# Optimization experiments

Measured on AMD Instinct MI355X. Metric: run time of the kernel, lower is better.

The kernel has to match this reference:

```python
import jax, jax.numpy as jnp
import numpy as np

HEADS = 24
HEAD_DIM = 128
HIDDEN = HEADS * HEAD_DIM          # 3072
MLP_DIM = int(HIDDEN * 4.0)        # 12288
EPS = 1e-6


def _layernorm(x, eps=EPS):
    mu = jnp.mean(x, axis=-1, keepdims=True)
    var = jnp.mean(jnp.square(x - mu), axis=-1, keepdims=True)
    return (x - mu) * jax.lax.rsqrt(var + eps)


def _rmsnorm(x, w, eps=EPS):
    var = jnp.mean(jnp.square(x), axis=-1, keepdims=True)
    return x * jax.lax.rsqrt(var + eps) * w


def _apply_rope_transposed(x, freqs_cis):
    # x: [B, S_img, H, Dh]; freqs_cis: [S_img, 2*Dh]
    cos, sin = jnp.split(freqs_cis[:, None, :], 2, axis=-1)  # each [S_img, 1, Dh]
    xr = x.reshape(*x.shape[:-1], -1, 2)                      # interleaved pairs
    x_real, x_imag = xr[..., 0], xr[..., 1]
    x_rot = jnp.stack([-x_imag, x_real], axis=-1).reshape(x.shape)
    return x * cos + x_rot * sin


def setup_inputs() -> dict:
    key = jax.random.key(0)
    ks = jax.random.split(key, 20)
    B, S_IMG, S_TXT = 1, 2048, 256
    s = 0.02
    inp = {
        "hidden_states": jax.random.normal(ks[0], (B, S_IMG, HIDDEN), jnp.float32),
        "encoder_hidden_states": jax.random.normal(ks[1], (B, S_TXT, HIDDEN), jnp.float32),
        "temb": jax.random.normal(ks[2], (B, HIDDEN), jnp.float32),
        "freqs_cis": jax.random.uniform(ks[3], (S_IMG, 2 * HEAD_DIM), jnp.float32),
        # AdaLN: Linear(hidden, 3*hidden)
        "w_norm": jax.random.normal(ks[4], (HIDDEN, 3 * HIDDEN), jnp.float32) * s,
        "b_norm": jnp.zeros((3 * HIDDEN,), jnp.float32),
        # attention projections (bias=True)
        "wq": jax.random.normal(ks[5], (HIDDEN, HIDDEN), jnp.float32) * s,
        "bq": jnp.zeros((HIDDEN,), jnp.float32),
        "wk": jax.random.normal(ks[6], (HIDDEN, HIDDEN), jnp.float32) * s,
        "bk": jnp.zeros((HIDDEN,), jnp.float32),
        "wv": jax.random.normal(ks[7], (HIDDEN, HIDDEN), jnp.float32) * s,
        "bv": jnp.zeros((HIDDEN,), jnp.float32),
        # QK RMSNorm weights over head_dim
        "nq_w": jnp.ones((HEAD_DIM,), jnp.float32),
        "nk_w": jnp.ones((HEAD_DIM,), jnp.float32),
        # parallel MLP branch
        "w_mlp": jax.random.normal(ks[8], (HIDDEN, MLP_DIM), jnp.float32) * s,
        "b_mlp": jnp.zeros((MLP_DIM,), jnp.float32),
        # proj_out: Linear(hidden + mlp_dim, hidden)
        "w_out": jax.random.normal(ks[9], (HIDDEN + MLP_DIM, HIDDEN), jnp.float32) * s,
        "b_out": jnp.zeros((HIDDEN,), jnp.float32),
    }
    return inp


def reference(hidden_states, encoder_hidden_states, temb, freqs_cis,
              w_norm, b_norm, wq, bq, wk, bk, wv, bv, nq_w, nk_w,
              w_mlp, b_mlp, w_out, b_out):
    B = hidden_states.shape[0]
    T = encoder_hidden_states.shape[1]  # text_seq_length

    x = jnp.concatenate([hidden_states, encoder_hidden_states], axis=1)  # [B,S,D]
    residual = x

    # AdaLayerNormZeroSingle
    emb = jax.nn.silu(temb) @ w_norm + b_norm          # [B, 3D]
    emb = emb[:, None, :]                              # [B, 1, 3D]
    shift, scale, gate = jnp.split(emb, 3, axis=-1)    # each [B,1,D]
    nx = _layernorm(x) * (1.0 + scale) + shift         # [B,S,D]

    # parallel MLP branch
    mlp = jax.nn.gelu(nx @ w_mlp + b_mlp, approximate=True)  # [B,S,MLP]

    # attention: q/k/v over full (img+txt) normed sequence
    q = (nx @ wq + bq).reshape(B, -1, HEADS, HEAD_DIM)
    k = (nx @ wk + bk).reshape(B, -1, HEADS, HEAD_DIM)
    v = (nx @ wv + bv).reshape(B, -1, HEADS, HEAD_DIM)
    q = _rmsnorm(q, nq_w)
    k = _rmsnorm(k, nk_w)

    # transposed RoPE on image tokens only
    q = jnp.concatenate([_apply_rope_transposed(q[:, :-T], freqs_cis), q[:, -T:]], axis=1)
    k = jnp.concatenate([_apply_rope_transposed(k[:, :-T], freqs_cis), k[:, -T:]], axis=1)

    # full (non-varlen) scaled dot-product attention
    scores = jnp.einsum("bqhd,bkhd->bhqk", q, k) / np.sqrt(HEAD_DIM).astype(np.float32)
    probs = jax.nn.softmax(scores, axis=-1)
    attn = jnp.einsum("bhqk,bkhd->bqhd", probs, v).reshape(B, -1, HIDDEN)

    # concat attention + mlp, project, gated residual
    h = jnp.concatenate([attn, mlp], axis=2)           # [B,S,D+MLP]
    h = gate * (h @ w_out + b_out) + residual          # [B,S,D]

    return h[:, :-T, :], h[:, -T:, :]
```

## Files before the change

### kernel.cpp

```cpp
#include <hip/hip_runtime.h>
#include <hip/hip_bf16.h>

typedef unsigned short u16;
typedef short s16x8 __attribute__((ext_vector_type(8)));
typedef float f32x4 __attribute__((ext_vector_type(4)));
typedef int   i32x4 __attribute__((ext_vector_type(4)));
typedef int   i32x2 __attribute__((ext_vector_type(2)));
typedef u16   u16x4 __attribute__((ext_vector_type(4)));
typedef unsigned int u32;
typedef u32   u32x2 __attribute__((ext_vector_type(2)));

#define HEADS  24
#define HD     128
#define HIDDEN 3072
#define MLPD   12288
#define NTOK   2304
#define SIMG   2048
#define NEMB   9216
#define CATD   15360
#define QKVD   9216
#define FUSEN  21504
#define LN_EPS 1e-6f
#define MB     9

__device__ __forceinline__ u16 f2us(float f){
  __hip_bfloat16 h = __float2bfloat16(f);
  return *reinterpret_cast<u16*>(&h);
}
__device__ __forceinline__ float us2f(u16 u){
  __hip_bfloat16 h;
  *reinterpret_cast<u16*>(&h) = u;
  return __bfloat162float(h);
}
__device__ __forceinline__ float gelu_tanh(float x){
  float y = 0.7978845608028654f*(x + 0.044715f*x*x*x);
  y = fminf(fmaxf(y, -12.f), 12.f);
  float e = __expf(-2.f*y);
  float t = (1.f - e) / (1.f + e);
  return 0.5f*x*(1.0f + t);
}
__device__ __forceinline__ void gload16(const u16* g, u16* l){
  __builtin_amdgcn_global_load_lds(
      (const __attribute__((address_space(1))) void*)g,
      (__attribute__((address_space(3))) void*)l, 16, 0, 0);
}
#define BAR() do{ asm volatile("":::"memory"); __builtin_amdgcn_s_barrier(); asm volatile("":::"memory"); }while(0)
#define LGKM0() asm volatile("s_waitcnt lgkmcnt(0)":::"memory")
#define VMW_(n) asm volatile("s_waitcnt vmcnt(" #n ")":::"memory")
#define VMW(n) VMW_(n)

__global__ __launch_bounds__(256)
void emb_partial(const float* __restrict__ temb, const float* __restrict__ wn,
                 float* __restrict__ partial)
{
  __shared__ float ls[384];
  int tid = threadIdx.x;
  int kb = blockIdx.y * 384;
  for (int i = tid; i < 384; i += 256){
    float t = temb[kb + i];
    ls[i] = t / (1.0f + __expf(-t));
  }
  __syncthreads();
  int j = blockIdx.x*256 + tid;
  const float* wp = wn + (size_t)kb*NEMB + j;
  float acc = 0.f;
  #pragma unroll 8
  for (int i = 0; i < 384; i++){ acc = fmaf(ls[i], wp[0], acc); wp += NEMB; }
  partial[blockIdx.y*NEMB + j] = acc;
}

__global__ __launch_bounds__(256)
void emb_reduce(const float* __restrict__ partial, const float* __restrict__ bn,
                float* __restrict__ emb)
{
  int j = blockIdx.x*256 + threadIdx.x;
  float s = bn[j];
  #pragma unroll
  for (int r = 0; r < 8; r++) s += partial[r*NEMB + j];
  emb[j] = s;
}

__global__ __launch_bounds__(256)
void ln_mod(const float* __restrict__ hs, const float* __restrict__ ehs,
            const float* __restrict__ emb, u16* __restrict__ nx)
{
  int row = blockIdx.x;
  const float* x = (row < SIMG) ? hs + (size_t)row*HIDDEN
                                : ehs + (size_t)(row - SIMG)*HIDDEN;
  int tid = threadIdx.x;
  float vals[12];
  float s = 0.f, ss = 0.f;
  #pragma unroll
  for (int i = 0; i < 3; i++){
    float4 v = *reinterpret_cast<const float4*>(x + i*1024 + tid*4);
    vals[i*4+0]=v.x; vals[i*4+1]=v.y; vals[i*4+2]=v.z; vals[i*4+3]=v.w;
    s += v.x+v.y+v.z+v.w;
    ss += v.x*v.x + v.y*v.y + v.z*v.z + v.w*v.w;
  }
  #pragma unroll
  for (int d = 1; d < 64; d <<= 1){ s += __shfl_xor(s, d); ss += __shfl_xor(ss, d); }
  __shared__ float red[8];
  if ((tid & 63) == 0){ red[tid>>6] = s; red[4 + (tid>>6)] = ss; }
  __syncthreads();
  s  = red[0]+red[1]+red[2]+red[3];
  ss = red[4]+red[5]+red[6]+red[7];
  float mu = s * (1.0f/HIDDEN);
  float var = ss * (1.0f/HIDDEN) - mu*mu;
  float rs = rsqrtf(var + LN_EPS);
  #pragma unroll
  for (int i = 0; i < 3; i++){
    int col = i*1024 + tid*4;
    u16x4 o;
    #pragma unroll
    for (int j = 0; j < 4; j++){
      float nv = (vals[i*4+j] - mu) * rs;
      float outv = nv * (1.0f + emb[HIDDEN + col + j]) + emb[col + j];
      o[j] = f2us(outv);
    }
    *reinterpret_cast<u16x4*>(nx + (size_t)row*HIDDEN + col) = o;
  }
}

__global__ __launch_bounds__(256)
void transpose_w(const float* __restrict__ W, u16* __restrict__ Wt,
                 int K, int N, int ldt, int noff)
{
  __shared__ float t[64][65];
  const int tid = threadIdx.x;
  const int kb = blockIdx.y * 64, nb = blockIdx.x * 64;
  #pragma unroll
  for (int i = 0; i < 4; i++){
    int row = (tid >> 4) + i*16;
    int c4  = (tid & 15) * 4;
    float4 v = *reinterpret_cast<const float4*>(W + (size_t)(kb+row)*N + nb + c4);
    t[row][c4] = v.x; t[row][c4+1] = v.y; t[row][c4+2] = v.z; t[row][c4+3] = v.w;
  }
  __syncthreads();
  int n  = tid >> 2;
  int kc = (tid & 3) * 16;
  u16 tmp[16];
  #pragma unroll
  for (int j = 0; j < 16; j++) tmp[j] = f2us(t[kc+j][n]);
  u16* dst = Wt + (size_t)(noff + nb + n)*ldt + kb + kc;
  *reinterpret_cast<i32x4*>(dst)     = *reinterpret_cast<const i32x4*>(tmp);
  *reinterpret_cast<i32x4*>(dst + 8) = *reinterpret_cast<const i32x4*>(tmp + 8);
}

template<int EPI>
__global__ __launch_bounds__(512, 2)
void gemm8(const u16* __restrict__ A_, int lda,
           const u16* __restrict__ Bt_, int ldb,
           int K, int N, int kspl,
           const float* __restrict__ b0, const float* __restrict__ b1,
           const float* __restrict__ b2, const float* __restrict__ b3,
           u16* __restrict__ qkvo, u16* __restrict__ hcat,
           float* __restrict__ outf)
{
  extern __shared__ __align__(16) u16 lds[];
  const int tid = threadIdx.x, lane = tid & 63, wid = tid >> 6;
  const int l15 = lane & 15, lhi = lane >> 4;
  const int wm = wid >> 2, wn = wid & 3;
  const int NKH = K / 32;

  const u16* Ag = A_  + (size_t)blockIdx.z * kspl;
  const u16* Bg = Bt_ + (size_t)blockIdx.z * kspl;

  const int nwg = gridDim.x;
  int orig = blockIdx.x;
  int qq = nwg >> 3, rr = nwg & 7;
  int xcd = orig & 7, loc = orig >> 3;
  int wg = (xcd < rr ? xcd*(qq+1) : rr*(qq+1) + (xcd-rr)*qq) + loc;
  const int m0 = (wg % MB) * 256;
  const int n0 = (wg / MB) * 256;

  const u16 *gA0, *gA1, *gB0, *gB1;
  {
    size_t offA[2], offB[2];
    #pragma unroll
    for (int q = 0; q < 2; q++){
      int Lb = q*8192 + tid*16;
      int r  = Lb >> 7;
      int gp = (Lb >> 4) & 7;
      int g  = gp ^ (r & 7);
      int row = 2*r + (g >> 2);
      int ke  = (g & 3) * 8;
      offA[q] = (size_t)(m0 + row)*lda + ke;
      offB[q] = (size_t)(n0 + row)*ldb + ke;
    }
    gA0 = Ag + offA[0]; gA1 = Ag + offA[1];
    gB0 = Bg + offB[0]; gB1 = Bg + offB[1];
  }
  u16* dA0 = lds + tid*8;
  u16* dA1 = lds + 4096 + tid*8;
  u16* dB0 = lds + 32768 + tid*8;
  u16* dB1 = lds + 36864 + tid*8;

  const char *pa0, *pb0;
  {
    const char* LB = (const char*)lds;
    int Ra = wm*128 + l15;
    pa0 = LB + (Ra>>1)*128 + (((((Ra&1)<<2)|lhi) ^ ((Ra>>1)&7))*16);
    int Rb = wn*64 + l15;
    pb0 = LB + 65536 + (Rb>>1)*128 + (((((Rb&1)<<2)|lhi) ^ ((Rb>>1)&7))*16);
  }

  f32x4 acc[8][4];
  #pragma unroll
  for (int i = 0; i < 8; i++)
    #pragma unroll
    for (int j = 0; j < 4; j++){ f32x4 z = {0.f,0.f,0.f,0.f}; acc[i][j] = z; }

  #define LD8(P_) (*reinterpret_cast<const s16x8*>(P_))
  #define MFMA_ALL(AF_, BF_) do{                                               \
    _Pragma("unroll") for (int a_=0;a_<8;a_++)                                 \
      _Pragma("unroll") for (int nf_=0;nf_<4;nf_++)                            \
        acc[a_][nf_] = __builtin_amdgcn_mfma_f32_16x16x32_bf16(                \
            (AF_)[a_], (BF_)[nf_], acc[a_][nf_], 0, 0, 0); }while(0)

  #define PHASEP(RP_,SP_,DOI_,GOFF_,VN_) do{                                   \
    s16x8 af[8], bf[4];                                                        \
    af[0] = LD8(pa0 + (RP_)*16384);                                            \
    _Pragma("unroll") for (int i_=0;i_<4;i_++)                                 \
      bf[i_] = LD8(pb0 + (RP_)*16384 + i_*1024);                               \
    _Pragma("unroll") for (int i_=1;i_<8;i_++)                                 \
      af[i_] = LD8(pa0 + (RP_)*16384 + (i_>>2)*4096 + (i_&3)*1024);            \
    if (DOI_){                                                                 \
      gload16(gA0+(GOFF_), dA0+(SP_)*8192); gload16(gA1+(GOFF_), dA1+(SP_)*8192);\
      gload16(gB0+(GOFF_), dB0+(SP_)*8192); gload16(gB1+(GOFF_), dB1+(SP_)*8192);\
    }                                                                          \
    __builtin_amdgcn_s_setprio(1);                                             \
    MFMA_ALL(af, bf);                                                          \
    __builtin_amdgcn_s_setprio(0);                                             \
    LGKM0();                                                                   \
    VMW(VN_);                                                                  \
    BAR();                                                                     \
  }while(0)

  gload16(gA0,    dA0);        gload16(gA1,    dA1);
  gload16(gB0,    dB0);        gload16(gB1,    dB1);
  gload16(gA0+32, dA0+8192);   gload16(gA1+32, dA1+8192);
  gload16(gB0+32, dB0+8192);   gload16(gB1+32, dB1+8192);
  gload16(gA0+64, dA0+16384);  gload16(gA1+64, dA1+16384);
  gload16(gB0+64, dB0+16384);  gload16(gB1+64, dB1+16384);
  VMW(8);
  BAR();

  const int nblk = NKH >> 3;
  for (int b = 0; b < nblk - 1; b++){
    PHASEP(0,3,1, 96,8); PHASEP(1,0,1,128,8); PHASEP(2,1,1,160,8); PHASEP(3,2,1,192,8);
    PHASEP(0,3,1,224,8); PHASEP(1,0,1,256,8); PHASEP(2,1,1,288,8); PHASEP(3,2,1,320,8);
    gA0 += 256; gA1 += 256; gB0 += 256; gB1 += 256;
  }
  PHASEP(0,3,1, 96,8); PHASEP(1,0,1,128,8); PHASEP(2,1,1,160,8); PHASEP(3,2,1,192,8);
  PHASEP(0,3,1,224,8); PHASEP(1,0,0,  0,4); PHASEP(2,1,0,  0,0); PHASEP(3,2,0,  0,0);

  #undef PHASEP
  #undef MFMA_ALL
  #undef LD8

  #pragma unroll
  for (int a = 0; a < 8; a++){
    #pragma unroll
    for (int nf = 0; nf < 4; nf++){
      int col = n0 + wn*64 + nf*16 + l15;
      #pragma unroll
      for (int r = 0; r < 4; r++){
        int row = m0 + wm*128 + a*16 + lhi*4 + r;
        float v = acc[a][nf][r];
        if constexpr (EPI == 0){
          if (col < QKVD){
            const float* bp = b0; int c = col;
            if (c >= 6144){ bp = b2; c -= 6144; }
            else if (c >= 3072){ bp = b1; c -= 3072; }
            qkvo[(size_t)row*QKVD + col] = f2us(v + bp[c]);
          } else {
            int c2 = col - QKVD;
            hcat[(size_t)row*CATD + HIDDEN + c2] = f2us(gelu_tanh(v + b3[c2]));
          }
        } else {
          outf[(size_t)blockIdx.z*NTOK*HIDDEN + (size_t)row*HIDDEN + col] = v;
        }
      }
    }
  }
}

__global__ __launch_bounds__(256)
void reduce_out(const float* __restrict__ part, const float* __restrict__ bout,
                const float* __restrict__ emb,
                const float* __restrict__ hs, const float* __restrict__ ehs,
                float* __restrict__ outp)
{
  int row = blockIdx.x;
  const float* res = (row < SIMG) ? hs + (size_t)row*HIDDEN
                                  : ehs + (size_t)(row - SIMG)*HIDDEN;
  #pragma unroll
  for (int i = 0; i < 3; i++){
    int col = i*1024 + threadIdx.x*4;
    float4 a = *reinterpret_cast<const float4*>(part + (size_t)row*HIDDEN + col);
    float4 b = *reinterpret_cast<const float4*>(part + (size_t)NTOK*HIDDEN + (size_t)row*HIDDEN + col);
    float4 rr = *reinterpret_cast<const float4*>(res + col);
    float4 bb = *reinterpret_cast<const float4*>(bout + col);
    float4 gg = *reinterpret_cast<const float4*>(emb + 2*HIDDEN + col);
    float4 o;
    o.x = gg.x*(a.x+b.x+bb.x) + rr.x;
    o.y = gg.y*(a.y+b.y+bb.y) + rr.y;
    o.z = gg.z*(a.z+b.z+bb.z) + rr.z;
    o.w = gg.w*(a.w+b.w+bb.w) + rr.w;
    *reinterpret_cast<float4*>(outp + (size_t)row*HIDDEN + col) = o;
  }
}

__global__ __launch_bounds__(256)
void qk_post(u16* __restrict__ qkv,
             const float* __restrict__ nqw, const float* __restrict__ nkw,
             const float* __restrict__ fc)
{
  int rid = blockIdx.x*4 + (threadIdx.x >> 6);
  int lane = threadIdx.x & 63;
  int isK = rid >= NTOK*HEADS;
  int r = isK ? rid - NTOK*HEADS : rid;
  int token = r / HEADS, head = r % HEADS;
  u16* p = qkv + (size_t)token*QKVD + (isK ? HIDDEN : 0) + head*HD + lane*2;
  unsigned int u = *reinterpret_cast<unsigned int*>(p);
  float v0 = us2f((u16)(u & 0xffff));
  float v1 = us2f((u16)(u >> 16));
  float ss = v0*v0 + v1*v1;
  #pragma unroll
  for (int d = 1; d < 64; d <<= 1) ss += __shfl_xor(ss, d);
  float rs = rsqrtf(ss * (1.0f/HD) + LN_EPS);
  const float* wv = isK ? nkw : nqw;
  v0 *= rs * wv[lane*2];
  v1 *= rs * wv[lane*2+1];
  if (token < SIMG){
    const float* f = fc + (size_t)token*(2*HD);
    float c0 = f[lane*2],      c1 = f[lane*2+1];
    float s0 = f[HD + lane*2], s1 = f[HD + lane*2+1];
    float o0 = v0*c0 - v1*s0;
    float o1 = v1*c1 + v0*s1;
    v0 = o0; v1 = o1;
  }
  unsigned int uo = (unsigned int)f2us(v0) | ((unsigned int)f2us(v1) << 16);
  *reinterpret_cast<unsigned int*>(p) = uo;
}

__global__ __launch_bounds__(512)
void attn_kernel(const u16* __restrict__ qkv, u16* __restrict__ hcat)
{
  __shared__ __align__(16) u16 Ks[64][136];
  __shared__ __align__(16) u16 Vt[128][72];
  __shared__ __align__(16) u16 Ps[128][72];

  const int tid = threadIdx.x, lane = tid & 63, w = tid >> 6;
  const int head = blockIdx.y;
  const int l15 = lane & 15, lhi = lane >> 4;
  const int q0 = blockIdx.x * 128;
  const float scale = 0.08838834764831845f;

  s16x8 qf[4];
  {
    const u16* qrow = qkv + (size_t)(q0 + w*16 + l15)*QKVD + head*HD;
    #pragma unroll
    for (int ks = 0; ks < 4; ks++)
      qf[ks] = *reinterpret_cast<const s16x8*>(qrow + ks*32 + lhi*8);
  }

  int krow[2], kd0[2];
  #pragma unroll
  for (int i = 0; i < 2; i++){ int c = tid + 512*i; krow[i] = c >> 4; kd0[i] = (c & 15)*8; }
  const int vd0   = (tid & 31) * 4;
  const int vbase = (tid >> 5) * 4;
  char* vwp = (char*)(&Vt[0][0]) + vd0*144 + (((vbase>>3) ^ ((vd0>>3)&7))*16) + (vbase&7)*2;

  i32x4 kr0, kr1;
  i32x2 vr0, vr1, vr2, vr3;
  {
    const u16* kbp = qkv + HIDDEN + (size_t)head*HD;
    const u16* vbp = qkv + 2*HIDDEN + (size_t)head*HD;
    kr0 = *reinterpret_cast<const i32x4*>(kbp + (size_t)(krow[0])*QKVD + kd0[0]);
    kr1 = *reinterpret_cast<const i32x4*>(kbp + (size_t)(krow[1])*QKVD + kd0[1]);
    vr0 = *reinterpret_cast<const i32x2*>(vbp + (size_t)(vbase+0)*QKVD + vd0);
    vr1 = *reinterpret_cast<const i32x2*>(vbp + (size_t)(vbase+1)*QKVD + vd0);
    vr2 = *reinterpret_cast<const i32x2*>(vbp + (size_t)(vbase+2)*QKVD + vd0);
    vr3 = *reinterpret_cast<const i32x2*>(vbp + (size_t)(vbase+3)*QKVD + vd0);
  }

  f32x4 O[8];
  #pragma unroll
  for (int i = 0; i < 8; i++){ f32x4 z = {0.f,0.f,0.f,0.f}; O[i] = z; }
  float mrow[4], lrow[4];
  #pragma unroll
  for (int r = 0; r < 4; r++){ mrow[r] = -1e30f; lrow[r] = 0.f; }

  for (int kv0 = 0; kv0 < NTOK; kv0 += 64){
    *reinterpret_cast<i32x4*>(&Ks[krow[0]][kd0[0]]) = kr0;
    *reinterpret_cast<i32x4*>(&Ks[krow[1]][kd0[1]]) = kr1;
    #pragma unroll
    for (int dd = 0; dd < 4; dd++){
      u32 a0 = (u32)(dd & 1 ? ((u32)vr0[dd>>1]) >> 16 : ((u32)vr0[dd>>1]) & 0xffff);
      u32 a1 = (u32)(dd & 1 ? ((u32)vr1[dd>>1]) >> 16 : ((u32)vr1[dd>>1]) & 0xffff);
      u32 a2 = (u32)(dd & 1 ? ((u32)vr2[dd>>1]) >> 16 : ((u32)vr2[dd>>1]) & 0xffff);
      u32 a3 = (u32)(dd & 1 ? ((u32)vr3[dd>>1]) >> 16 : ((u32)vr3[dd>>1]) & 0xffff);
      u32x2 pk; pk[0] = a0 | (a1 << 16); pk[1] = a2 | (a3 << 16);
      *reinterpret_cast<u32x2*>(vwp + dd*144) = pk;
    }
    __syncthreads();

    if (kv0 + 64 < NTOK){
      const u16* kbp = qkv + (size_t)(kv0+64)*QKVD + HIDDEN + (size_t)head*HD;
      const u16* vbp = qkv + (size_t)(kv0+64)*QKVD + 2*HIDDEN + (size_t)head*HD;
      kr0 = *reinterpret_cast<const i32x4*>(kbp + (size_t)(krow[0])*QKVD + kd0[0]);
      kr1 = *reinterpret_cast<const i32x4*>(kbp + (size_t)(krow[1])*QKVD + kd0[1]);
      vr0 = *reinterpret_cast<const i32x2*>(vbp + (size_t)(vbase+0)*QKVD + vd0);
      vr1 = *reinterpret_cast<const i32x2*>(vbp + (size_t)(vbase+1)*QKVD + vd0);
      vr2 = *reinterpret_cast<const i32x2*>(vbp + (size_t)(vbase+2)*QKVD + vd0);
      vr3 = *reinterpret_cast<const i32x2*>(vbp + (size_t)(vbase+3)*QKVD + vd0);
    }

    f32x4 S[4];
    #pragma unroll
    for (int nf = 0; nf < 4; nf++){ f32x4 z = {0.f,0.f,0.f,0.f}; S[nf] = z; }
    #pragma unroll
    for (int ks = 0; ks < 4; ks++){
      #pragma unroll
      for (int nf = 0; nf < 4; nf++){
        s16x8 b = *reinterpret_cast<const s16x8*>(&Ks[nf*16 + l15][ks*32 + lhi*8]);
        S[nf] = __builtin_amdgcn_mfma_f32_16x16x32_bf16(qf[ks], b, S[nf], 0, 0, 0);
      }
    }
    #pragma unroll
    for (int nf = 0; nf < 4; nf++)
      #pragma unroll
      for (int r = 0; r < 4; r++) S[nf][r] *= scale;

    float fsc[4];
    #pragma unroll
    for (int r = 0; r < 4; r++){
      float mx = -1e30f;
      #pragma unroll
      for (int nf = 0; nf < 4; nf++) mx = fmaxf(mx, S[nf][r]);
      #pragma unroll
      for (int d = 1; d < 16; d <<= 1) mx = fmaxf(mx, __shfl_xor(mx, d));
      float mn = fmaxf(mrow[r], mx);
      float f = __expf(mrow[r] - mn);
      mrow[r] = mn; fsc[r] = f;
      float lsum = 0.f;
      int prow = w*16 + lhi*4 + r;
      #pragma unroll
      for (int nf = 0; nf < 4; nf++){
        float pvl = __expf(S[nf][r] - mn);
        lsum += pvl;
        int pcol = nf*16 + l15;
        int col = (((pcol>>3) ^ (prow&7)) << 3) | (pcol & 7);
        Ps[prow][col] = f2us(pvl);
      }
      #pragma unroll
      for (int d = 1; d < 16; d <<= 1) lsum += __shfl_xor(lsum, d);
      lrow[r] = lrow[r]*f + lsum;
    }
    #pragma unroll
    for (int nf = 0; nf < 8; nf++)
      #pragma unroll
      for (int r = 0; r < 4; r++) O[nf][r] *= fsc[r];

    #pragma unroll
    for (int ks = 0; ks < 2; ks++){
      int prow = w*16 + l15;
      int cb = ((ks*4 + lhi) ^ (prow & 7)) << 3;
      s16x8 a = *reinterpret_cast<const s16x8*>(&Ps[prow][cb]);
      #pragma unroll
      for (int nf = 0; nf < 8; nf++){
        int d = nf*16 + l15;
        int vb = ((ks*4 + lhi) ^ ((d>>3)&7)) << 3;
        s16x8 b = *reinterpret_cast<const s16x8*>(&Vt[d][vb]);
        O[nf] = __builtin_amdgcn_mfma_f32_16x16x32_bf16(a, b, O[nf], 0, 0, 0);
      }
    }
    __syncthreads();
  }

  #pragma unroll
  for (int nf = 0; nf < 8; nf++){
    #pragma unroll
    for (int r = 0; r < 4; r++){
      int row = q0 + w*16 + lhi*4 + r;
      int col = head*HD + nf*16 + l15;
      hcat[(size_t)row*CATD + col] = f2us(O[nf][r] / lrow[r]);
    }
  }
}

extern "C" void kernel_launch(void* const* d_in, const int* in_sizes, int n_in,
                              void* d_out, int out_size, void* d_ws, size_t ws_size,
                              hipStream_t stream)
{
  const float* hs    = (const float*)d_in[0];
  const float* ehs   = (const float*)d_in[1];
  const float* temb  = (const float*)d_in[2];
  const float* fc    = (const float*)d_in[3];
  const float* wnorm = (const float*)d_in[4];
  const float* bnorm = (const float*)d_in[5];
  const float* wq    = (const float*)d_in[6];
  const float* bq    = (const float*)d_in[7];
  const float* wk    = (const float*)d_in[8];
  const float* bk    = (const float*)d_in[9];
  const float* wv    = (const float*)d_in[10];
  const float* bv    = (const float*)d_in[11];
  const float* nqw   = (const float*)d_in[12];
  const float* nkw   = (const float*)d_in[13];
  const float* wmlp  = (const float*)d_in[14];
  const float* bmlp  = (const float*)d_in[15];
  const float* wout  = (const float*)d_in[16];
  const float* bout  = (const float*)d_in[17];
  float* outp = (float*)d_out;

  char* ws = (char*)d_ws;
  float* emb  = (float*)ws;
  float* part = (float*)(ws + 36864);
  u16* nx     = (u16*)(ws + 36864 + 294912);
  u16* qkv    = nx  + (size_t)NTOK*HIDDEN;
  u16* hcat   = qkv + (size_t)NTOK*QKVD;
  u16* Wt     = hcat + (size_t)NTOK*CATD;
  float* partial = (float*)nx;

  hipFuncSetAttribute((const void*)gemm8<0>, hipFuncAttributeMaxDynamicSharedMemorySize, 131072);
  hipFuncSetAttribute((const void*)gemm8<1>, hipFuncAttributeMaxDynamicSharedMemorySize, 131072);

  emb_partial<<<dim3(36,8), 256, 0, stream>>>(temb, wnorm, part);
  emb_reduce<<<36, 256, 0, stream>>>(part, bnorm, emb);
  ln_mod<<<NTOK, 256, 0, stream>>>(hs, ehs, emb, nx);

  transpose_w<<<dim3(48,48), 256, 0, stream>>>(wq,   Wt, HIDDEN, HIDDEN, HIDDEN, 0);
  transpose_w<<<dim3(48,48), 256, 0, stream>>>(wk,   Wt, HIDDEN, HIDDEN, HIDDEN, HIDDEN);
  transpose_w<<<dim3(48,48), 256, 0, stream>>>(wv,   Wt, HIDDEN, HIDDEN, HIDDEN, 2*HIDDEN);
  transpose_w<<<dim3(192,48), 256, 0, stream>>>(wmlp, Wt, HIDDEN, MLPD, HIDDEN, QKVD);

  gemm8<0><<<dim3((FUSEN/256)*MB, 1, 1), 512, 131072, stream>>>(
      nx, HIDDEN, Wt, HIDDEN, HIDDEN, FUSEN, 0,
      bq, bk, bv, bmlp, qkv, hcat, nullptr);

  transpose_w<<<dim3(48,240), 256, 0, stream>>>(wout, Wt, CATD, HIDDEN, CATD, 0);

  qk_post<<<(2*NTOK*HEADS)/4, 256, 0, stream>>>(qkv, nqw, nkw, fc);
  attn_kernel<<<dim3(NTOK/128, HEADS), 512, 0, stream>>>(qkv, hcat);

  gemm8<1><<<dim3((HIDDEN/256)*MB, 1, 2), 512, 131072, stream>>>(
      hcat, CATD, Wt, CATD, CATD/2, HIDDEN, CATD/2,
      nullptr, nullptr, nullptr, nullptr, nullptr, nullptr, partial);

  reduce_out<<<NTOK, 256, 0, stream>>>(partial, bout, emb, hs, ehs, outp);
}
```

Measured before the change: 952.3 us.

## Restructure GEMM main loop into quadrant-split ping-pong with 64-wide K tiles

Replaces the 4-stage 32-wide K pipeline with a double-buffered 64-wide K tile scheme. Each tile is split into four quadrant MFMA sub-phases (A-half by B-half), with LDS fragment reads and global-to-LDS staging interleaved between them. The aim is to overlap LDS reads and global loads with MFMA work at a finer grain and to cut register pressure for fragments. In exchange it adds more barriers per tile and a more delicate buffer-reuse schedule.

```diff
diff --git a/kernel.cpp b/kernel.cpp
--- a/kernel.cpp
+++ b/kernel.cpp
@@ -160,7 +160,7 @@
   const int tid = threadIdx.x, lane = tid & 63, wid = tid >> 6;
   const int l15 = lane & 15, lhi = lane >> 4;
   const int wm = wid >> 2, wn = wid & 3;
-  const int NKH = K / 32;
+  const int NT = K / 64;
 
   const u16* Ag = A_  + (size_t)blockIdx.z * kspl;
   const u16* Bg = Bt_ + (size_t)blockIdx.z * kspl;
@@ -190,10 +190,6 @@
     gA0 = Ag + offA[0]; gA1 = Ag + offA[1];
     gB0 = Bg + offB[0]; gB1 = Bg + offB[1];
   }
-  u16* dA0 = lds + tid*8;
-  u16* dA1 = lds + 4096 + tid*8;
-  u16* dB0 = lds + 32768 + tid*8;
-  u16* dB1 = lds + 36864 + tid*8;
 
   const char *pa0, *pb0;
   {
@@ -210,53 +206,96 @@
     #pragma unroll
     for (int j = 0; j < 4; j++){ f32x4 z = {0.f,0.f,0.f,0.f}; acc[i][j] = z; }
 
+  s16x8 aset[8], bset[4];
+
   #define LD8(P_) (*reinterpret_cast<const s16x8*>(P_))
-  #define MFMA_ALL(AF_, BF_) do{                                               \
-    _Pragma("unroll") for (int a_=0;a_<8;a_++)                                 \
-      _Pragma("unroll") for (int nf_=0;nf_<4;nf_++)                            \
-        acc[a_][nf_] = __builtin_amdgcn_mfma_f32_16x16x32_bf16(                \
-            (AF_)[a_], (BF_)[nf_], acc[a_][nf_], 0, 0, 0); }while(0)
-
-  #define PHASEP(RP_,SP_,DOI_,GOFF_,VN_) do{                                   \
-    s16x8 af[8], bf[4];                                                        \
-    af[0] = LD8(pa0 + (RP_)*16384);                                            \
-    _Pragma("unroll") for (int i_=0;i_<4;i_++)                                 \
-      bf[i_] = LD8(pb0 + (RP_)*16384 + i_*1024);                               \
-    _Pragma("unroll") for (int i_=1;i_<8;i_++)                                 \
-      af[i_] = LD8(pa0 + (RP_)*16384 + (i_>>2)*4096 + (i_&3)*1024);            \
-    if (DOI_){                                                                 \
-      gload16(gA0+(GOFF_), dA0+(SP_)*8192); gload16(gA1+(GOFF_), dA1+(SP_)*8192);\
-      gload16(gB0+(GOFF_), dB0+(SP_)*8192); gload16(gB1+(GOFF_), dB1+(SP_)*8192);\
-    }                                                                          \
-    __builtin_amdgcn_s_setprio(1);                                             \
-    MFMA_ALL(af, bf);                                                          \
-    __builtin_amdgcn_s_setprio(0);                                             \
-    LGKM0();                                                                   \
-    VMW(VN_);                                                                  \
-    BAR();                                                                     \
+  #define READ_A(QM_, PP_) do{                                                 \
+    _Pragma("unroll") for (int kh_=0;kh_<2;kh_++)                              \
+      _Pragma("unroll") for (int mf_=0;mf_<4;mf_++)                            \
+        aset[kh_*4+mf_] = LD8(pa0 + ((PP_)*2+kh_)*16384 + (QM_)*4096 + mf_*1024);}while(0)
+  #define READ_B(QN_, PP_) do{                                                 \
+    _Pragma("unroll") for (int kh_=0;kh_<2;kh_++)                              \
+      _Pragma("unroll") for (int nf_=0;nf_<2;nf_++)                            \
+        bset[kh_*2+nf_] = LD8(pb0 + ((PP_)*2+kh_)*16384 + (QN_)*2048 + nf_*1024);}while(0)
+  #define MM16(QM_, QN_) do{                                                   \
+    _Pragma("unroll") for (int kh_=0;kh_<2;kh_++)                              \
+      _Pragma("unroll") for (int mf_=0;mf_<4;mf_++)                            \
+        _Pragma("unroll") for (int nf_=0;nf_<2;nf_++)                          \
+          acc[(QM_)*4+mf_][(QN_)*2+nf_] = __builtin_amdgcn_mfma_f32_16x16x32_bf16(\
+              aset[kh_*4+mf_], bset[kh_*2+nf_], acc[(QM_)*4+mf_][(QN_)*2+nf_],0,0,0);}while(0)
+  #define STGA(GOFF_, RB_) do{ gload16(gA0+(GOFF_), lds+(RB_)+tid*8);          \
+                               gload16(gA1+(GOFF_), lds+(RB_)+4096+tid*8); }while(0)
+  #define STGB(GOFF_, RB_) do{ gload16(gB0+(GOFF_), lds+(RB_)+tid*8);          \
+                               gload16(gB1+(GOFF_), lds+(RB_)+4096+tid*8); }while(0)
+  #define PRIO1() __builtin_amdgcn_s_setprio(1)
+  #define PRIO0() __builtin_amdgcn_s_setprio(0)
+
+  #define TILE_FULL(P_) do{                                                    \
+                                                              \
+    READ_A(0,P_); READ_B(0,P_);                                                \
+    STGA((P_)?160:96, (P_)?8192:24576);                                        \
+    STGB((P_)?128:64, (P_)?32768:49152);                                       \
+    BAR(); LGKM0(); PRIO1(); MM16(0,0); PRIO0(); BAR();                        \
+                                                              \
+    READ_B(1,P_);                                                              \
+    STGB((P_)?160:96, (P_)?40960:57344);                                       \
+    BAR(); LGKM0(); PRIO1(); MM16(0,1); PRIO0(); BAR();                        \
+                                                              \
+    READ_A(1,P_);                                                              \
+    BAR(); LGKM0(); PRIO1(); MM16(1,1); PRIO0(); BAR();                        \
+                                                              \
+    READ_B(0,P_);                                                              \
+    STGA((P_)?192:128, (P_)?16384:0);                                          \
+    BAR(); LGKM0(); PRIO1(); MM16(1,0); PRIO0(); VMW(2); BAR();                \
   }while(0)
 
-  gload16(gA0,    dA0);        gload16(gA1,    dA1);
-  gload16(gB0,    dB0);        gload16(gB1,    dB1);
-  gload16(gA0+32, dA0+8192);   gload16(gA1+32, dA1+8192);
-  gload16(gB0+32, dB0+8192);   gload16(gB1+32, dB1+8192);
-  gload16(gA0+64, dA0+16384);  gload16(gA1+64, dA1+16384);
-  gload16(gB0+64, dB0+16384);  gload16(gB1+64, dB1+16384);
-  VMW(8);
+  STGA(0, 0);
+  STGA(32, 8192);
+  STGB(0, 32768);
+  STGB(32, 40960);
+  STGA(64, 16384);
+  VMW(2);
   BAR();
 
-  const int nblk = NKH >> 3;
-  for (int b = 0; b < nblk - 1; b++){
-    PHASEP(0,3,1, 96,8); PHASEP(1,0,1,128,8); PHASEP(2,1,1,160,8); PHASEP(3,2,1,192,8);
-    PHASEP(0,3,1,224,8); PHASEP(1,0,1,256,8); PHASEP(2,1,1,288,8); PHASEP(3,2,1,320,8);
-    gA0 += 256; gA1 += 256; gB0 += 256; gB1 += 256;
-  }
-  PHASEP(0,3,1, 96,8); PHASEP(1,0,1,128,8); PHASEP(2,1,1,160,8); PHASEP(3,2,1,192,8);
-  PHASEP(0,3,1,224,8); PHASEP(1,0,0,  0,4); PHASEP(2,1,0,  0,0); PHASEP(3,2,0,  0,0);
-
-  #undef PHASEP
-  #undef MFMA_ALL
+  const int npair = (NT - 2) >> 1;
+  for (int pr = 0; pr < npair; pr++){
+    TILE_FULL(0);
+    TILE_FULL(1);
+    gA0 += 128; gA1 += 128; gB0 += 128; gB1 += 128;
+  }
+  {
+    READ_A(0,0); READ_B(0,0);
+    STGA(96, 24576);
+    STGB(64, 49152);
+    BAR(); LGKM0(); PRIO1(); MM16(0,0); PRIO0(); BAR();
+    READ_B(1,0);
+    STGB(96, 57344);
+    BAR(); LGKM0(); PRIO1(); MM16(0,1); PRIO0(); BAR();
+    READ_A(1,0);
+    BAR(); LGKM0(); PRIO1(); MM16(1,1); PRIO0(); BAR();
+    READ_B(0,0);
+    BAR(); LGKM0(); PRIO1(); MM16(1,0); PRIO0(); VMW(0); BAR();
+  }
+  {
+    READ_A(0,1); READ_B(0,1);
+    BAR(); LGKM0(); PRIO1(); MM16(0,0); PRIO0(); BAR();
+    READ_B(1,1);
+    BAR(); LGKM0(); PRIO1(); MM16(0,1); PRIO0(); BAR();
+    READ_A(1,1);
+    BAR(); LGKM0(); PRIO1(); MM16(1,1); PRIO0(); BAR();
+    READ_B(0,1);
+    LGKM0(); PRIO1(); MM16(1,0); PRIO0();
+  }
+
+  #undef TILE_FULL
+  #undef STGA
+  #undef STGB
+  #undef MM16
+  #undef READ_A
+  #undef READ_B
   #undef LD8
+  #undef PRIO1
+  #undef PRIO0
 
   #pragma unroll
   for (int a = 0; a < 8; a++){
```

Result: no change. 951.9 us (-0.0%).

## Quantize fused QKV+MLP GEMM to int8 with per-row and per-column scales

Applied to the files above, without the earlier changes.

Switches the big fused QKV/MLP projection from bf16 MFMA to int8 MFMA (16x16x64). LayerNorm output is quantized per row with a max-abs scale, and the weights are quantized per output column after a new column-max reduction pass. Results are dequantized in the epilogue. This roughly halves operand bandwidth and doubles MFMA throughput for the largest GEMM. In exchange it adds column-max kernels and risks accuracy loss from 8-bit quantization of activations and weights.

```diff
diff --git a/kernel.cpp b/kernel.cpp
--- a/kernel.cpp
+++ b/kernel.cpp
@@ -22,6 +22,7 @@
 #define FUSEN  21504
 #define LN_EPS 1e-6f
 #define MB     9
+#define INV127SQ (1.0f/16129.0f)
 
 __device__ __forceinline__ u16 f2us(float f){
   __hip_bfloat16 h = __float2bfloat16(f);
@@ -39,7 +40,11 @@
   float t = (1.f - e) / (1.f + e);
   return 0.5f*x*(1.0f + t);
 }
-__device__ __forceinline__ void gload16(const u16* g, u16* l){
+__device__ __forceinline__ int q8i(float x, float s){
+  int q = __float2int_rn(x*s);
+  return max(-127, min(127, q));
+}
+__device__ __forceinline__ void gload16(const void* g, void* l){
   __builtin_amdgcn_global_load_lds(
       (const __attribute__((address_space(1))) void*)g,
       (__attribute__((address_space(3))) void*)l, 16, 0, 0);
@@ -82,7 +87,8 @@
 
 __global__ __launch_bounds__(256)
 void ln_mod(const float* __restrict__ hs, const float* __restrict__ ehs,
-            const float* __restrict__ emb, u16* __restrict__ nx)
+            const float* __restrict__ emb, char* __restrict__ nx,
+            float* __restrict__ arow)
 {
   int row = blockIdx.x;
   const float* x = (row < SIMG) ? hs + (size_t)row*HIDDEN
@@ -107,23 +113,64 @@
   float mu = s * (1.0f/HIDDEN);
   float var = ss * (1.0f/HIDDEN) - mu*mu;
   float rs = rsqrtf(var + LN_EPS);
+
+  float mx = 1e-8f;
   #pragma unroll
   for (int i = 0; i < 3; i++){
     int col = i*1024 + tid*4;
-    u16x4 o;
     #pragma unroll
     for (int j = 0; j < 4; j++){
       float nv = (vals[i*4+j] - mu) * rs;
       float outv = nv * (1.0f + emb[HIDDEN + col + j]) + emb[col + j];
-      o[j] = f2us(outv);
-    }
-    *reinterpret_cast<u16x4*>(nx + (size_t)row*HIDDEN + col) = o;
-  }
-}
-
-__global__ __launch_bounds__(256)
-void transpose_w(const float* __restrict__ W, u16* __restrict__ Wt,
-                 int K, int N, int ldt, int noff)
+      vals[i*4+j] = outv;
+      mx = fmaxf(mx, fabsf(outv));
+    }
+  }
+  #pragma unroll
+  for (int d = 1; d < 64; d <<= 1) mx = fmaxf(mx, __shfl_xor(mx, d));
+  __shared__ float redm[4];
+  if ((tid & 63) == 0) redm[tid>>6] = mx;
+  __syncthreads();
+  mx = fmaxf(fmaxf(redm[0], redm[1]), fmaxf(redm[2], redm[3]));
+  if (tid == 0) arow[row] = mx;
+  float sq = 127.0f / mx;
+
+  #pragma unroll
+  for (int i = 0; i < 3; i++){
+    int col = i*1024 + tid*4;
+    u32 pk = 0;
+    #pragma unroll
+    for (int j = 0; j < 4; j++)
+      pk |= ((u32)(unsigned char)(char)q8i(vals[i*4+j], sq)) << (8*j);
+    *reinterpret_cast<u32*>(nx + (size_t)row*HIDDEN + col) = pk;
+  }
+}
+
+__global__ __launch_bounds__(256)
+void wcolmax_part(const float* __restrict__ W, float* __restrict__ wpart,
+                  int K, int N, int noff)
+{
+  int n = blockIdx.x*256 + threadIdx.x;
+  int kq = K >> 2;
+  const float* p = W + (size_t)blockIdx.y*kq*N + n;
+  float m = 1e-8f;
+  #pragma unroll 8
+  for (int k = 0; k < kq; k++){ m = fmaxf(m, fabsf(*p)); p += N; }
+  wpart[blockIdx.y*FUSEN + noff + n] = m;
+}
+
+__global__ __launch_bounds__(256)
+void wcolmax_fin(const float* __restrict__ wpart, float* __restrict__ wcol)
+{
+  int n = blockIdx.x*256 + threadIdx.x;
+  wcol[n] = fmaxf(fmaxf(wpart[n], wpart[FUSEN+n]),
+                  fmaxf(wpart[2*FUSEN+n], wpart[3*FUSEN+n]));
+}
+
+__global__ __launch_bounds__(256)
+void transpose_w_i8(const float* __restrict__ W, char* __restrict__ Wt,
+                    int K, int N, int ldt, int noff,
+                    const float* __restrict__ wcol)
 {
   __shared__ float t[64][65];
   const int tid = threadIdx.x;
@@ -138,6 +185,37 @@
   __syncthreads();
   int n  = tid >> 2;
   int kc = (tid & 3) * 16;
+  float sq = 127.0f / wcol[noff + nb + n];
+  u32 w0=0,w1=0,w2=0,w3=0;
+  #pragma unroll
+  for (int j = 0; j < 4; j++)  w0 |= ((u32)(unsigned char)(char)q8i(t[kc+j][n],    sq)) << (8*j);
+  #pragma unroll
+  for (int j = 0; j < 4; j++)  w1 |= ((u32)(unsigned char)(char)q8i(t[kc+4+j][n],  sq)) << (8*j);
+  #pragma unroll
+  for (int j = 0; j < 4; j++)  w2 |= ((u32)(unsigned char)(char)q8i(t[kc+8+j][n],  sq)) << (8*j);
+  #pragma unroll
+  for (int j = 0; j < 4; j++)  w3 |= ((u32)(unsigned char)(char)q8i(t[kc+12+j][n], sq)) << (8*j);
+  i32x4 o; o[0]=(int)w0; o[1]=(int)w1; o[2]=(int)w2; o[3]=(int)w3;
+  *reinterpret_cast<i32x4*>(Wt + (size_t)(noff + nb + n)*ldt + kb + kc) = o;
+}
+
+__global__ __launch_bounds__(256)
+void transpose_w(const float* __restrict__ W, u16* __restrict__ Wt,
+                 int K, int N, int ldt, int noff)
+{
+  __shared__ float t[64][65];
+  const int tid = threadIdx.x;
+  const int kb = blockIdx.y * 64, nb = blockIdx.x * 64;
+  #pragma unroll
+  for (int i = 0; i < 4; i++){
+    int row = (tid >> 4) + i*16;
+    int c4  = (tid & 15) * 4;
+    float4 v = *reinterpret_cast<const float4*>(W + (size_t)(kb+row)*N + nb + c4);
+    t[row][c4] = v.x; t[row][c4+1] = v.y; t[row][c4+2] = v.z; t[row][c4+3] = v.w;
+  }
+  __syncthreads();
+  int n  = tid >> 2;
+  int kc = (tid & 3) * 16;
   u16 tmp[16];
   #pragma unroll
   for (int j = 0; j < 16; j++) tmp[j] = f2us(t[kc+j][n]);
@@ -146,14 +224,136 @@
   *reinterpret_cast<i32x4*>(dst + 8) = *reinterpret_cast<const i32x4*>(tmp + 8);
 }
 
-template<int EPI>
+__global__ __launch_bounds__(512, 2)
+void gemm_i8(const char* __restrict__ A_, int lda,
+             const char* __restrict__ Bt_, int ldb,
+             const float* __restrict__ arow, const float* __restrict__ wcol,
+             const float* __restrict__ b0, const float* __restrict__ b1,
+             const float* __restrict__ b2, const float* __restrict__ b3,
+             u16* __restrict__ qkvo, u16* __restrict__ hcat)
+{
+  extern __shared__ __align__(16) char ldsc[];
+  const int tid = threadIdx.x, lane = tid & 63, wid = tid >> 6;
+  const int l15 = lane & 15, lhi = lane >> 4;
+  const int wm = wid >> 2, wn = wid & 3;
+  const int NT = HIDDEN / 64;
+
+  const int nwg = gridDim.x;
+  int orig = blockIdx.x;
+  int qq = nwg >> 3, rr = nwg & 7;
+  int xcd = orig & 7, loc = orig >> 3;
+  int wg = (xcd < rr ? xcd*(qq+1) : rr*(qq+1) + (xcd-rr)*qq) + loc;
+  const int m0 = (wg % MB) * 256;
+  const int n0 = (wg / MB) * 256;
+
+  const char *gAlo, *gAhi, *gBlo, *gBhi;
+  {
+    int r = tid >> 2;
+    int gs = (tid & 3) ^ (r & 3) ^ ((r >> 2) & 3);
+    gAlo = A_  + (size_t)(m0 + r)*lda + gs*16;
+    gAhi = A_  + (size_t)(m0 + 128 + r)*lda + gs*16;
+    gBlo = Bt_ + (size_t)(n0 + r)*ldb + gs*16;
+    gBhi = Bt_ + (size_t)(n0 + 128 + r)*ldb + gs*16;
+  }
+  char* dst16 = ldsc + tid*16;
+
+  const char *paw, *pbw;
+  {
+    int gsw = lhi ^ (l15 & 3) ^ ((l15 >> 2) & 3);
+    paw = ldsc + wm*8192 + l15*64 + gsw*16;
+    pbw = ldsc + 49152 + (wn>>1)*8192 + (wn&1)*4096 + l15*64 + gsw*16;
+  }
+
+  i32x4 acc[8][4];
+  #pragma unroll
+  for (int i = 0; i < 8; i++)
+    #pragma unroll
+    for (int j = 0; j < 4; j++){ i32x4 z = {0,0,0,0}; acc[i][j] = z; }
+
+  i32x4 aset[4], bset[2];
+
+  #define RD_A(P_,Q_) do{ _Pragma("unroll") for (int i_=0;i_<4;i_++)           \
+      aset[i_] = *reinterpret_cast<const i32x4*>(paw + (P_)*16384 + ((Q_)*4+i_)*1024); }while(0)
+  #define RD_B(P_,H_) do{ _Pragma("unroll") for (int i_=0;i_<2;i_++)           \
+      bset[i_] = *reinterpret_cast<const i32x4*>(pbw + (P_)*16384 + ((H_)*2+i_)*1024); }while(0)
+  #define MM8(Q_,H_) do{ _Pragma("unroll") for (int mf_=0;mf_<4;mf_++)         \
+      _Pragma("unroll") for (int nf_=0;nf_<2;nf_++)                            \
+        acc[(Q_)*4+mf_][(H_)*2+nf_] = __builtin_amdgcn_mfma_i32_16x16x64_i8(   \
+            aset[mf_], bset[nf_], acc[(Q_)*4+mf_][(H_)*2+nf_], 0, 0, 0); }while(0)
+  #define PRIO1() __builtin_amdgcn_s_setprio(1)
+  #define PRIO0() __builtin_amdgcn_s_setprio(0)
+
+  #define TILE_I8(P_,DOI_,DOV_,GOFF_) do{                                      \
+    constexpr int PS_ = ((P_)+2)%3;                                            \
+    RD_A(P_,0); RD_B(P_,0);                                                    \
+    if (DOI_){ gload16(gAlo+(GOFF_), dst16 + PS_*16384);                       \
+               gload16(gAhi+(GOFF_), dst16 + PS_*16384 + 8192); }              \
+    PRIO1(); MM8(0,0); PRIO0(); LGKM0(); BAR();                                \
+    RD_B(P_,1);                                                                \
+    if (DOI_){ gload16(gBlo+(GOFF_), dst16 + 49152 + PS_*16384);               \
+               gload16(gBhi+(GOFF_), dst16 + 49152 + PS_*16384 + 8192); }      \
+    PRIO1(); MM8(0,1); PRIO0(); LGKM0(); BAR();                                \
+    RD_A(P_,1);                                                                \
+    PRIO1(); MM8(1,1); PRIO0(); LGKM0(); BAR();                                \
+    RD_B(P_,0);                                                                \
+    PRIO1(); MM8(1,0); PRIO0(); LGKM0();                                       \
+    if ((DOV_)==1) VMW(4);                                                     \
+    if ((DOV_)==2) VMW(0);                                                     \
+    BAR();                                                                     \
+  }while(0)
+
+  gload16(gAlo,    dst16);          gload16(gAhi,    dst16 + 8192);
+  gload16(gBlo,    dst16 + 49152);  gload16(gBhi,    dst16 + 57344);
+  gload16(gAlo+64, dst16 + 16384);  gload16(gAhi+64, dst16 + 24576);
+  gload16(gBlo+64, dst16 + 65536);  gload16(gBhi+64, dst16 + 73728);
+  VMW(4);
+  BAR();
+
+  for (int m = 0; m < NT/3 - 1; m++){
+    TILE_I8(0,1,1,128);
+    TILE_I8(1,1,1,192);
+    TILE_I8(2,1,1,256);
+    gAlo += 192; gAhi += 192; gBlo += 192; gBhi += 192;
+  }
+  TILE_I8(0,1,1,128);
+  TILE_I8(1,0,2,0);
+  TILE_I8(2,0,0,0);
+
+  #undef TILE_I8
+  #undef MM8
+  #undef RD_A
+  #undef RD_B
+  #undef PRIO1
+  #undef PRIO0
+
+  #pragma unroll
+  for (int a = 0; a < 8; a++){
+    #pragma unroll
+    for (int nf = 0; nf < 4; nf++){
+      int col = n0 + wn*64 + nf*16 + l15;
+      float wsc = wcol[col] * INV127SQ;
+      #pragma unroll
+      for (int r = 0; r < 4; r++){
+        int row = m0 + wm*128 + a*16 + lhi*4 + r;
+        float v = (float)acc[a][nf][r] * arow[row] * wsc;
+        if (col < QKVD){
+          const float* bp = b0; int c = col;
+          if (c >= 6144){ bp = b2; c -= 6144; }
+          else if (c >= 3072){ bp = b1; c -= 3072; }
+          qkvo[(size_t)row*QKVD + col] = f2us(v + bp[c]);
+        } else {
+          int c2 = col - QKVD;
+          hcat[(size_t)row*CATD + HIDDEN + c2] = f2us(gelu_tanh(v + b3[c2]));
+        }
+      }
+    }
+  }
+}
+
 __global__ __launch_bounds__(512, 2)
 void gemm8(const u16* __restrict__ A_, int lda,
            const u16* __restrict__ Bt_, int ldb,
            int K, int N, int kspl,
-           const float* __restrict__ b0, const float* __restrict__ b1,
-           const float* __restrict__ b2, const float* __restrict__ b3,
-           u16* __restrict__ qkvo, u16* __restrict__ hcat,
            float* __restrict__ outf)
 {
   extern __shared__ __align__(16) u16 lds[];
@@ -266,20 +466,7 @@
       #pragma unroll
       for (int r = 0; r < 4; r++){
         int row = m0 + wm*128 + a*16 + lhi*4 + r;
-        float v = acc[a][nf][r];
-        if constexpr (EPI == 0){
-          if (col < QKVD){
-            const float* bp = b0; int c = col;
-            if (c >= 6144){ bp = b2; c -= 6144; }
-            else if (c >= 3072){ bp = b1; c -= 3072; }
-            qkvo[(size_t)row*QKVD + col] = f2us(v + bp[c]);
-          } else {
-            int c2 = col - QKVD;
-            hcat[(size_t)row*CATD + HIDDEN + c2] = f2us(gelu_tanh(v + b3[c2]));
-          }
-        } else {
-          outf[(size_t)blockIdx.z*NTOK*HIDDEN + (size_t)row*HIDDEN + col] = v;
-        }
+        outf[(size_t)blockIdx.z*NTOK*HIDDEN + (size_t)row*HIDDEN + col] = acc[a][nf][r];
       }
     }
   }
@@ -515,38 +702,47 @@
   float* outp = (float*)d_out;
 
   char* ws = (char*)d_ws;
-  float* emb  = (float*)ws;
-  float* part = (float*)(ws + 36864);
-  u16* nx     = (u16*)(ws + 36864 + 294912);
-  u16* qkv    = nx  + (size_t)NTOK*HIDDEN;
-  u16* hcat   = qkv + (size_t)NTOK*QKVD;
-  u16* Wt     = hcat + (size_t)NTOK*CATD;
-  float* partial = (float*)nx;
-
-  hipFuncSetAttribute((const void*)gemm8<0>, hipFuncAttributeMaxDynamicSharedMemorySize, 131072);
-  hipFuncSetAttribute((const void*)gemm8<1>, hipFuncAttributeMaxDynamicSharedMemorySize, 131072);
+  float* emb   = (float*)ws;
+  float* part  = (float*)(ws + 36864);
+  float* arow  = (float*)(ws + 331776);
+  float* wcol  = (float*)(ws + 340992);
+  float* wpart = (float*)(ws + 427008);
+  char*  nx8   = ws + 771072;
+  u16*   qkv   = (u16*)(ws + 7848960);
+  u16*   hcat  = (u16*)(ws + 57394176);
+  char*  wreg  = ws + 128173056;
+  char*  wt8   = wreg;
+  u16*   wtb   = (u16*)wreg;
+  float* partial = (float*)nx8;
+
+  hipFuncSetAttribute((const void*)gemm_i8, hipFuncAttributeMaxDynamicSharedMemorySize, 98304);
+  hipFuncSetAttribute((const void*)gemm8,   hipFuncAttributeMaxDynamicSharedMemorySize, 131072);
 
   emb_partial<<<dim3(36,8), 256, 0, stream>>>(temb, wnorm, part);
   emb_reduce<<<36, 256, 0, stream>>>(part, bnorm, emb);
-  ln_mod<<<NTOK, 256, 0, stream>>>(hs, ehs, emb, nx);
-
-  transpose_w<<<dim3(48,48), 256, 0, stream>>>(wq,   Wt, HIDDEN, HIDDEN, HIDDEN, 0);
-  transpose_w<<<dim3(48,48), 256, 0, stream>>>(wk,   Wt, HIDDEN, HIDDEN, HIDDEN, HIDDEN);
-  transpose_w<<<dim3(48,48), 256, 0, stream>>>(wv,   Wt, HIDDEN, HIDDEN, HIDDEN, 2*HIDDEN);
-  transpose_w<<<dim3(192,48), 256, 0, stream>>>(wmlp, Wt, HIDDEN, MLPD, HIDDEN, QKVD);
-
-  gemm8<0><<<dim3((FUSEN/256)*MB, 1, 1), 512, 131072, stream>>>(
-      nx, HIDDEN, Wt, HIDDEN, HIDDEN, FUSEN, 0,
-      bq, bk, bv, bmlp, qkv, hcat, nullptr);
-
-  transpose_w<<<dim3(48,240), 256, 0, stream>>>(wout, Wt, CATD, HIDDEN, CATD, 0);
+  ln_mod<<<NTOK, 256, 0, stream>>>(hs, ehs, emb, nx8, arow);
+
+  wcolmax_part<<<dim3(12,4), 256, 0, stream>>>(wq,   wpart, HIDDEN, HIDDEN, 0);
+  wcolmax_part<<<dim3(12,4), 256, 0, stream>>>(wk,   wpart, HIDDEN, HIDDEN, HIDDEN);
+  wcolmax_part<<<dim3(12,4), 256, 0, stream>>>(wv,   wpart, HIDDEN, HIDDEN, 2*HIDDEN);
+  wcolmax_part<<<dim3(48,4), 256, 0, stream>>>(wmlp, wpart, HIDDEN, MLPD, QKVD);
+  wcolmax_fin<<<84, 256, 0, stream>>>(wpart, wcol);
+
+  transpose_w_i8<<<dim3(48,48), 256, 0, stream>>>(wq,   wt8, HIDDEN, HIDDEN, HIDDEN, 0,        wcol);
+  transpose_w_i8<<<dim3(48,48), 256, 0, stream>>>(wk,   wt8, HIDDEN, HIDDEN, HIDDEN, HIDDEN,   wcol);
+  transpose_w_i8<<<dim3(48,48), 256, 0, stream>>>(wv,   wt8, HIDDEN, HIDDEN, HIDDEN, 2*HIDDEN, wcol);
+  transpose_w_i8<<<dim3(192,48), 256, 0, stream>>>(wmlp, wt8, HIDDEN, MLPD, HIDDEN, QKVD,      wcol);
+
+  gemm_i8<<<dim3((FUSEN/256)*MB, 1, 1), 512, 98304, stream>>>(
+      nx8, HIDDEN, wt8, HIDDEN, arow, wcol, bq, bk, bv, bmlp, qkv, hcat);
+
+  transpose_w<<<dim3(48,240), 256, 0, stream>>>(wout, wtb, CATD, HIDDEN, CATD, 0);
 
   qk_post<<<(2*NTOK*HEADS)/4, 256, 0, stream>>>(qkv, nqw, nkw, fc);
   attn_kernel<<<dim3(NTOK/128, HEADS), 512, 0, stream>>>(qkv, hcat);
 
-  gemm8<1><<<dim3((HIDDEN/256)*MB, 1, 2), 512, 131072, stream>>>(
-      hcat, CATD, Wt, CATD, CATD/2, HIDDEN, CATD/2,
-      nullptr, nullptr, nullptr, nullptr, nullptr, nullptr, partial);
+  gemm8<<<dim3((HIDDEN/256)*MB, 1, 2), 512, 131072, stream>>>(
+      hcat, CATD, wtb, CATD, CATD/2, HIDDEN, CATD/2, partial);
 
   reduce_out<<<NTOK, 256, 0, stream>>>(partial, bout, emb, hs, ehs, outp);
 }
```

Result: slower. 1.049 ms (+10.1%).
